# Kernel tuning notes

Hardware: AMD Instinct MI355X
Metric: run time of the kernel (lower is better)

The kernel has to match this reference:

```python
import jax, jax.numpy as jnp
import numpy as np

N_NODES = 50000
N_EDGES = 800000
NUM_GRAPHS = 128
FEAT = 128
HID = 64
NUM_LAYERS = 3
OUT = 2
K = 30
LATENT = HID * NUM_LAYERS + 1  # 193 = conv1 kernel size & stride


def _lin(k, i, o):
    s = 1.0 / np.sqrt(i)
    return jax.random.uniform(k, (i, o), jnp.float32, -s, s)


def setup_inputs() -> dict:
    key = jax.random.key(0)
    ks = jax.random.split(key, 16)
    x = jax.random.normal(ks[0], (N_NODES, FEAT), jnp.float32)
    edge_index = jax.random.randint(ks[1], (2, N_EDGES), 0, N_NODES, dtype=jnp.int64)
    batch = jnp.sort(jax.random.randint(ks[2], (N_NODES,), 0, NUM_GRAPHS, dtype=jnp.int64))
    w0 = _lin(ks[3], FEAT, HID); b0 = jnp.zeros((HID,), jnp.float32)
    w1 = _lin(ks[4], HID, HID);  b1 = jnp.zeros((HID,), jnp.float32)
    w2 = _lin(ks[5], HID, HID);  b2 = jnp.zeros((HID,), jnp.float32)
    w3 = _lin(ks[6], HID, 1);    b3 = jnp.zeros((1,), jnp.float32)
    conv1_w = jax.random.normal(ks[7], (16, 1, LATENT), jnp.float32) * (1.0 / np.sqrt(LATENT))
    conv1_b = jnp.zeros((16,), jnp.float32)
    conv2_w = jax.random.normal(ks[8], (32, 16, 5), jnp.float32) * (1.0 / np.sqrt(16 * 5))
    conv2_b = jnp.zeros((32,), jnp.float32)
    dense_dim = (int((K - 2) / 2 + 1) - 5 + 1) * 32  # 352
    lin1_w = _lin(ks[9], dense_dim, 256); lin1_b = jnp.zeros((256,), jnp.float32)
    lin2_w = _lin(ks[10], 256, OUT);      lin2_b = jnp.zeros((OUT,), jnp.float32)
    return dict(x=x, edge_index=edge_index, batch=batch,
                w0=w0, b0=b0, w1=w1, b1=b1, w2=w2, b2=b2, w3=w3, b3=b3,
                conv1_w=conv1_w, conv1_b=conv1_b, conv2_w=conv2_w, conv2_b=conv2_b,
                lin1_w=lin1_w, lin1_b=lin1_b, lin2_w=lin2_w, lin2_b=lin2_b)


def _gcn(h_in, w, b, src, dst, norm, n):
    # GCNConv: out_i = sum_j d_i^-1/2 d_j^-1/2 (x_j W) over A+I, plus bias
    h = h_in @ w
    msg = h[src] * norm[:, None]  # gather over edges (incl. self loops)
    return jax.ops.segment_sum(msg, dst, num_segments=n) + b


def _sort_pool(x, batch, k, g):
    # per-graph descending sort on last channel, top-k, zero-pad
    n, d = x.shape
    order = jnp.lexsort((-x[:, -1], batch))  # primary: batch asc, secondary: last feat desc
    xs, bs = x[order], batch[order]
    counts = jax.ops.segment_sum(jnp.ones((n,), jnp.int32), batch, num_segments=g)
    starts = jnp.cumsum(counts) - counts
    rank = jnp.arange(n) - starts[bs]
    slot = jnp.where(rank < k, rank, k)  # overflow nodes dumped in slot k (discarded)
    out = jnp.zeros((g, k + 1, d), x.dtype).at[bs, slot].set(xs)
    return out[:, :k].reshape(g, k * d)


def _conv1d(z, w, stride):
    return jax.lax.conv_general_dilated(z, w, window_strides=(stride,), padding='VALID',
                                        dimension_numbers=('NCH', 'OIH', 'NCH'))


def reference(x, edge_index, batch, w0, b0, w1, b1, w2, b2, w3, b3,
              conv1_w, conv1_b, conv2_w, conv2_b, lin1_w, lin1_b, lin2_w, lin2_b):
    n = x.shape[0]
    loop = jnp.arange(n, dtype=edge_index.dtype)
    src = jnp.concatenate([edge_index[0], loop])
    dst = jnp.concatenate([edge_index[1], loop])
    deg = jax.ops.segment_sum(jnp.ones_like(src, jnp.float32), dst, num_segments=n)
    dinv = jnp.where(deg > 0, jax.lax.rsqrt(deg), 0.0)
    norm = dinv[src] * dinv[dst]

    h1 = jnp.tanh(_gcn(x,  w0, b0, src, dst, norm, n))
    h2 = jnp.tanh(_gcn(h1, w1, b1, src, dst, norm, n))
    h3 = jnp.tanh(_gcn(h2, w2, b2, src, dst, norm, n))
    h4 = jnp.tanh(_gcn(h3, w3, b3, src, dst, norm, n))
    hcat = jnp.concatenate([h1, h2, h3, h4], axis=-1)  # [N, 193]

    p = _sort_pool(hcat, batch, K, NUM_GRAPHS)  # [G, K*193]
    z = p[:, None, :]                                   # [G, 1, K*193]
    z = jax.nn.relu(_conv1d(z, conv1_w, LATENT) + conv1_b[None, :, None])  # [G,16,K]
    g, c, l = z.shape
    z = z.reshape(g, c, l // 2, 2).max(axis=-1)         # MaxPool1d(2,2) -> [G,16,15]
    z = jax.nn.relu(_conv1d(z, conv2_w, 1) + conv2_b[None, :, None])       # [G,32,11]
    z = z.reshape(g, -1)                                # [G,352]
    z = jax.nn.relu(z @ lin1_w + lin1_b)
    # dropout is identity in eval mode
    return z @ lin2_w + lin2_b
```

## Files before the change

kernel.cpp:

```cpp
#include <hip/hip_runtime.h>
#include <math.h>

#define NGRAPH 128
#define KTOP 30
#define LATENT 193
#define HID 64

typedef unsigned short u16;

__global__ void k_zero(int* edeg, int n) {
    int i = blockIdx.x * blockDim.x + threadIdx.x;
    if (i < n) edeg[i] = 0;
}

template <bool SCALE>
__device__ __forceinline__ void gemm_tile(const float* __restrict__ A,
                                          const float* __restrict__ W,
                                          const float* __restrict__ dinv,
                                          float* __restrict__ Hs,
                                          int M, int K, int br,
                                          float (*As)[68], float (*Bs)[68]) {
    int tid = threadIdx.x;
    int tx = tid & 15, ty = tid >> 4;
    int kA = (tid & 7) * 4;
    int rA = tid >> 3;
    int kB = tid >> 3;
    int cB = (tid & 7) * 8;
    float c[4][4] = {};
    for (int k0 = 0; k0 < K; k0 += 32) {
#pragma unroll
        for (int it = 0; it < 2; ++it) {
            int row = it * 32 + rA;
            int grow = br + row;
            float4 v = make_float4(0.f, 0.f, 0.f, 0.f);
            if (grow < M) v = *(const float4*)(A + (size_t)grow * K + k0 + kA);
            As[kA + 0][row] = v.x;
            As[kA + 1][row] = v.y;
            As[kA + 2][row] = v.z;
            As[kA + 3][row] = v.w;
        }
        {
            const float* wp = W + (size_t)(k0 + kB) * 64 + cB;
            float4 v0 = *(const float4*)(wp);
            float4 v1 = *(const float4*)(wp + 4);
            *(float4*)&Bs[kB][cB] = v0;
            *(float4*)&Bs[kB][cB + 4] = v1;
        }
        __syncthreads();
#pragma unroll
        for (int kk = 0; kk < 32; ++kk) {
            float4 a4 = *(const float4*)&As[kk][ty * 4];
            float4 b4 = *(const float4*)&Bs[kk][tx * 4];
            c[0][0] += a4.x * b4.x; c[0][1] += a4.x * b4.y; c[0][2] += a4.x * b4.z; c[0][3] += a4.x * b4.w;
            c[1][0] += a4.y * b4.x; c[1][1] += a4.y * b4.y; c[1][2] += a4.y * b4.z; c[1][3] += a4.y * b4.w;
            c[2][0] += a4.z * b4.x; c[2][1] += a4.z * b4.y; c[2][2] += a4.z * b4.z; c[2][3] += a4.z * b4.w;
            c[3][0] += a4.w * b4.x; c[3][1] += a4.w * b4.y; c[3][2] += a4.w * b4.z; c[3][3] += a4.w * b4.w;
        }
        __syncthreads();
    }
#pragma unroll
    for (int i = 0; i < 4; i++) {
        int row = br + ty * 4 + i;
        if (row >= M) continue;
        float d = SCALE ? dinv[row] : 1.f;
        float4 o;
        o.x = c[i][0] * d; o.y = c[i][1] * d; o.z = c[i][2] * d; o.w = c[i][3] * d;
        *(float4*)(Hs + (size_t)row * HID + tx * 4) = o;
    }
}

__global__ __launch_bounds__(256) void k_gemm_hist(
        const float* __restrict__ A, const float* __restrict__ W,
        float* __restrict__ Hs, int M, int K, int NG,
        const int* __restrict__ dst, const int* __restrict__ batch,
        int* edeg, u16* __restrict__ rank, int* starts,
        int E, int n, int NH) {
    __shared__ float As[32][68];
    __shared__ float Bs[32][68];
    int bid = blockIdx.x;
    if ((bid & 1) == 0) {
        int gid = bid >> 1;
        if (gid >= NG) return;
        gemm_tile<false>(A, W, nullptr, Hs, M, K, gid * 64, As, Bs);
    } else {
        int fid = bid >> 1;
        if (fid >= NH) return;
        int t = threadIdx.x;
        int gi = fid * 256 + t;
        if (gi < n) {
            int b = batch[gi];
            if (gi == 0) {
                for (int g = 0; g <= b; g++) starts[g] = 0;
            } else {
                int pb = batch[gi - 1];
                for (int g = pb + 1; g <= b; g++) starts[g] = gi;
            }
            if (gi == n - 1) {
                for (int g = b + 1; g <= NGRAPH; g++) starts[g] = n;
            }
        }
        int base = fid * 1024;
#pragma unroll
        for (int k = 0; k < 4; k++) {
            int e = base + k * 256 + t;
            if (e < E) {
                int d = dst[e];
                rank[e] = (u16)atomicAdd(&edeg[d], 1);
            }
        }
    }
}

__global__ void k_scan1(const int* __restrict__ edeg, int* offs, int* bsum,
                        float* dinv, int n) {
    __shared__ int s[256];
    int t = threadIdx.x;
    int gi = blockIdx.x * 256 + t;
    int v = (gi < n) ? edeg[gi] : 0;
    if (gi < n) dinv[gi] = rsqrtf((float)(v + 1));
    s[t] = v;
    __syncthreads();
    for (int o = 1; o < 256; o <<= 1) {
        int add = (t >= o) ? s[t - o] : 0;
        __syncthreads();
        s[t] += add;
        __syncthreads();
    }
    if (gi < n) offs[gi] = s[t] - v;
    if (t == 255) bsum[blockIdx.x] = s[255];
}

__global__ void k_scan23(int* offs, const int* __restrict__ bsum,
                         int n, int E, int nb) {
    __shared__ int s[256];
    int t = threadIdx.x;
    int bid = blockIdx.x;
    int v = (t < nb) ? bsum[t] : 0;
    s[t] = v;
    __syncthreads();
    for (int o = 1; o < 256; o <<= 1) {
        int add = (t >= o) ? s[t - o] : 0;
        __syncthreads();
        s[t] += add;
        __syncthreads();
    }
    int boffv = (bid == 0) ? 0 : s[bid - 1];
    int gi = bid * 256 + t;
    if (gi < n) offs[gi] += boffv;
    if (gi == 0) offs[n] = E;
}

__global__ __launch_bounds__(256) void k_fill_scale(
        const int* __restrict__ src, const int* __restrict__ dst,
        const u16* __restrict__ rank, const int* __restrict__ offs,
        u16* __restrict__ csr, int E, int NF,
        float* __restrict__ Hs, const float* __restrict__ dinv, int n) {
    int bid = blockIdx.x;
    if (bid < NF) {
        int t = bid * 256 + threadIdx.x;
        int e0 = t * 4;
        if (e0 + 4 <= E) {
            int4 s4 = *(const int4*)(src + e0);
            int4 d4 = *(const int4*)(dst + e0);
            uint2 rv = *(const uint2*)(rank + e0);
            csr[offs[d4.x] + (rv.x & 0xffff)] = (u16)s4.x;
            csr[offs[d4.y] + (rv.x >> 16)]    = (u16)s4.y;
            csr[offs[d4.z] + (rv.y & 0xffff)] = (u16)s4.z;
            csr[offs[d4.w] + (rv.y >> 16)]    = (u16)s4.w;
        } else {
            for (int e = e0; e < E; e++)
                csr[offs[dst[e]] + rank[e]] = (u16)src[e];
        }
    } else {
        int idx = (bid - NF) * 256 + threadIdx.x;
        if (idx < n * HID) Hs[idx] *= dinv[idx >> 6];
    }
}

__global__ __launch_bounds__(256) void k_gemm(const float* __restrict__ A,
                                              const float* __restrict__ W,
                                              const float* __restrict__ dinv,
                                              float* __restrict__ Hs,
                                              int M, int K) {
    __shared__ float As[32][68];
    __shared__ float Bs[32][68];
    gemm_tile<true>(A, W, dinv, Hs, M, K, blockIdx.x * 64, As, Bs);
}

template <bool FUSE_TS>
__global__ __launch_bounds__(256) void k_agg(const float* __restrict__ Hs,
                                             const u16* __restrict__ csr,
                                             const int* __restrict__ offs,
                                             const float* __restrict__ dinv,
                                             const float* __restrict__ b,
                                             float* __restrict__ H, int n,
                                             const float* __restrict__ w3,
                                             float* __restrict__ ts) {
    int wid = threadIdx.x >> 6;
    int lane = threadIdx.x & 63;
    int node = blockIdx.x * 4 + wid;
    if (node >= n) return;
    float d = dinv[node];
    float acc = Hs[(size_t)node * HID + lane];
    int s = offs[node], e = offs[node + 1];
    int i = s;
    int ahead = (s + 7) & ~7;
    if (ahead > e) ahead = e;
    for (; i < ahead; i++) acc += Hs[(size_t)csr[i] * HID + lane];
    for (; i + 8 <= e; i += 8) {
        uint4 c8 = *(const uint4*)(csr + i);
        float v0 = Hs[(size_t)(c8.x & 0xffff) * HID + lane];
        float v1 = Hs[(size_t)(c8.x >> 16)    * HID + lane];
        float v2 = Hs[(size_t)(c8.y & 0xffff) * HID + lane];
        float v3 = Hs[(size_t)(c8.y >> 16)    * HID + lane];
        float v4 = Hs[(size_t)(c8.z & 0xffff) * HID + lane];
        float v5 = Hs[(size_t)(c8.z >> 16)    * HID + lane];
        float v6 = Hs[(size_t)(c8.w & 0xffff) * HID + lane];
        float v7 = Hs[(size_t)(c8.w >> 16)    * HID + lane];
        acc += ((v0 + v1) + (v2 + v3)) + ((v4 + v5) + (v6 + v7));
    }
    for (; i < e; i++) acc += Hs[(size_t)csr[i] * HID + lane];
    float h = tanhf(acc * d + b[lane]);
    H[(size_t)node * HID + lane] = h;
    if (FUSE_TS) {
        float v = h * w3[lane];
        for (int o = 32; o > 0; o >>= 1) v += __shfl_down(v, o, 64);
        if (lane == 0) ts[node] = v * d;
    }
}

__global__ __launch_bounds__(1024) void k_select_tail(
        const float* __restrict__ h1, const float* __restrict__ h2,
        const float* __restrict__ h3, const float* __restrict__ ts,
        const u16* __restrict__ csr, const int* __restrict__ offs,
        const float* __restrict__ dinv, const float* __restrict__ b3,
        const int* __restrict__ starts,
        const float* __restrict__ c1w, const float* __restrict__ c1b,
        const float* __restrict__ c2w, const float* __restrict__ c2b,
        const float* __restrict__ l1w, const float* __restrict__ l1b,
        const float* __restrict__ l2w, const float* __restrict__ l2b,
        float* __restrict__ out) {
    __shared__ float p[KTOP * LATENT];
    __shared__ float w1s[16 * LATENT];
    __shared__ float w2s[32 * 16 * 5];
    __shared__ float vv[2048];
    __shared__ int   pr[2048];
    __shared__ int   sel_s[KTOP];
    __shared__ float zpart[960];
    __shared__ float z1[16 * KTOP];
    __shared__ float z1p[16 * 15];
    __shared__ float flat[352];
    __shared__ float part[1024];
    __shared__ float y1[256];
    int g = blockIdx.x;
    int t = threadIdx.x;
    int s = starts[g];
    int c = starts[g + 1] - s;
    if (c > 2048) c = 2048;

    for (int i = t; i < 16 * LATENT; i += 1024) w1s[i] = c1w[i];
    for (int i = t; i < 32 * 16 * 5; i += 1024) w2s[i] = c2w[i];
    if (t < KTOP) sel_s[t] = -1;

    float bb = b3[0];
    for (int i = t; i < c; i += 1024) {
        int node = s + i;
        float acc = ts[node];
        int es = offs[node], ee = offs[node + 1];
        for (int j = es; j < ee; j++) acc += ts[csr[j]];
        vv[i] = tanhf(acc * dinv[node] + bb);
    }
    __syncthreads();

    int chalf = c >> 1;
    for (int i2 = t; i2 < 2 * c; i2 += 1024) {
        int i = i2 >> 1, half = i2 & 1;
        float vi = vv[i];
        int j0 = half ? chalf : 0;
        int j1 = half ? c : chalf;
        int r = 0;
        for (int j = j0; j < j1; j++) {
            float vj = vv[j];
            r += (vj > vi) || (vj == vi && j < i);
        }
        pr[i2] = r;
    }
    __syncthreads();
    for (int i = t; i < c; i += 1024) {
        int r = pr[2 * i] + pr[2 * i + 1];
        if (r < KTOP) sel_s[r] = s + i;
    }
    __syncthreads();

    for (int i = t; i < KTOP * LATENT; i += 1024) {
        int slot = i / LATENT;
        int j = i - slot * LATENT;
        int node = sel_s[slot];
        float v = 0.f;
        if (node >= 0) {
            if (j < 64)       v = h1[(size_t)node * HID + j];
            else if (j < 128) v = h2[(size_t)node * HID + j - 64];
            else if (j < 192) v = h3[(size_t)node * HID + j - 128];
            else              v = vv[node - s];
        }
        p[i] = v;
    }
    __syncthreads();
    if (t < 960) {
        int to = (t < 480) ? t : t - 480;
        int half = (t < 480) ? 0 : 1;
        int ch = to / KTOP, tt = to - ch * KTOP;
        const float* wp = &w1s[ch * LATENT];
        const float* pp = &p[tt * LATENT];
        int j0 = half ? 96 : 0;
        int j1 = half ? LATENT : 96;
        float sa = 0.f;
        for (int j = j0; j < j1; j++) sa += pp[j] * wp[j];
        zpart[t] = sa;
    }
    __syncthreads();
    if (t < 480) {
        int ch = t / KTOP, tt = t - ch * KTOP;
        z1[ch * KTOP + tt] = fmaxf(zpart[t] + zpart[480 + t] + c1b[ch], 0.f);
    }
    __syncthreads();
    if (t < 16 * 15) {
        int ch = t / 15, tt = t - ch * 15;
        z1p[t] = fmaxf(z1[ch * KTOP + 2 * tt], z1[ch * KTOP + 2 * tt + 1]);
    }
    __syncthreads();
    if (t < 32 * 11) {
        int c2 = t / 11, tt = t - c2 * 11;
        float sa = c2b[c2];
        for (int c1i = 0; c1i < 16; c1i++) {
            const float* wp = &w2s[(c2 * 16 + c1i) * 5];
            const float* zp = &z1p[c1i * 15 + tt];
#pragma unroll
            for (int dt = 0; dt < 5; dt++) sa += zp[dt] * wp[dt];
        }
        flat[c2 * 11 + tt] = fmaxf(sa, 0.f);
    }
    __syncthreads();
    {
        int o = t & 255, ch = t >> 8;
        int i0 = ch * 88, i1 = i0 + 88;
        float sa = 0.f;
        for (int i = i0; i < i1; i++) sa += flat[i] * l1w[(size_t)i * 256 + o];
        part[t] = sa;
    }
    __syncthreads();
    if (t < 256)
        y1[t] = fmaxf(part[t] + part[256 + t] + part[512 + t] + part[768 + t] + l1b[t], 0.f);
    __syncthreads();
    if (t < 128) {
        int o = t >> 6, lane = t & 63;
        float sa = 0.f;
        for (int i = lane; i < 256; i += 64) sa += y1[i] * l2w[(size_t)i * 2 + o];
        for (int off = 32; off > 0; off >>= 1) sa += __shfl_down(sa, off, 64);
        if (lane == 0) out[g * 2 + o] = sa + l2b[o];
    }
}

static inline char* align256(char* p) {
    return (char*)(((uintptr_t)p + 255) & ~(uintptr_t)255);
}

extern "C" void kernel_launch(void* const* d_in, const int* in_sizes, int n_in,
                              void* d_out, int out_size, void* d_ws, size_t ws_size,
                              hipStream_t stream) {
    const float* x     = (const float*)d_in[0];
    const int*  eidx   = (const int*)d_in[1];
    const int*  batch  = (const int*)d_in[2];
    const float* w0    = (const float*)d_in[3];
    const float* b0    = (const float*)d_in[4];
    const float* w1    = (const float*)d_in[5];
    const float* b1    = (const float*)d_in[6];
    const float* w2    = (const float*)d_in[7];
    const float* b2    = (const float*)d_in[8];
    const float* w3    = (const float*)d_in[9];
    const float* b3    = (const float*)d_in[10];
    const float* c1w   = (const float*)d_in[11];
    const float* c1b   = (const float*)d_in[12];
    const float* c2w   = (const float*)d_in[13];
    const float* c2b   = (const float*)d_in[14];
    const float* l1w   = (const float*)d_in[15];
    const float* l1b   = (const float*)d_in[16];
    const float* l2w   = (const float*)d_in[17];
    const float* l2b   = (const float*)d_in[18];

    int N = in_sizes[2];
    int E = in_sizes[1] / 2;
    int K0 = in_sizes[0] / N;
    const int* esrc = eidx;
    const int* edst = eidx + E;

    char* w = (char*)d_ws;
    float* dinv  = (float*)w;             w = align256(w + (size_t)N * 4);
    int*   edeg  = (int*)w;               w = align256(w + (size_t)N * 4);
    int*   offs  = (int*)w;               w = align256(w + (size_t)(N + 1) * 4);
    int*   bsum  = (int*)w;               w = align256(w + 1024);
    float* ts    = (float*)w;             w = align256(w + (size_t)N * 4);
    int* starts  = (int*)w;               w = align256(w + (NGRAPH + 1) * 4);
    u16* rank    = (u16*)w;               w = align256(w + (size_t)E * 2);
    u16* csr     = (u16*)w;               w = align256(w + (size_t)E * 2);
    float* Hs    = (float*)w;             w = align256(w + (size_t)N * HID * 4);
    float* h1    = (float*)w;             w = align256(w + (size_t)N * HID * 4);
    float* h2    = (float*)w;             w = align256(w + (size_t)N * HID * 4);
    float* h3    = (float*)w;             w = align256(w + (size_t)N * HID * 4);

    int nb = (N + 255) / 256;
    int NG = (N + 63) / 64;
    int NH = (E + 1023) / 1024;
    int NF = (E / 4 + 255) / 256 + 1;
    int NS = ((size_t)N * HID + 255) / 256;
    int agg_grid = (N + 3) / 4;

    k_zero<<<nb, 256, 0, stream>>>(edeg, N);

    int g1 = 2 * (NG > NH ? NG : NH);
    k_gemm_hist<<<g1, 256, 0, stream>>>(x, w0, Hs, N, K0, NG,
                                        edst, batch, edeg, rank, starts, E, N, NH);

    k_scan1<<<nb, 256, 0, stream>>>(edeg, offs, bsum, dinv, N);
    k_scan23<<<nb, 256, 0, stream>>>(offs, bsum, N, E, nb);

    k_fill_scale<<<NF + NS, 256, 0, stream>>>(esrc, edst, rank, offs, csr, E, NF,
                                              Hs, dinv, N);

    k_agg<false><<<agg_grid, 256, 0, stream>>>(Hs, csr, offs, dinv, b0, h1, N, nullptr, nullptr);
    k_gemm<<<NG, 256, 0, stream>>>(h1, w1, dinv, Hs, N, HID);
    k_agg<false><<<agg_grid, 256, 0, stream>>>(Hs, csr, offs, dinv, b1, h2, N, nullptr, nullptr);
    k_gemm<<<NG, 256, 0, stream>>>(h2, w2, dinv, Hs, N, HID);
    k_agg<true><<<agg_grid, 256, 0, stream>>>(Hs, csr, offs, dinv, b2, h3, N, w3, ts);

    k_select_tail<<<NGRAPH, 1024, 0, stream>>>(h1, h2, h3, ts, csr, offs, dinv, b3,
                                               starts,
                                               c1w, c1b, c2w, c2b,
                                               l1w, l1b, l2w, l2b,
                                               (float*)d_out);
}
```

Measured before the change: 282.2 us.

## Defer first-layer dinv scaling into aggregation and split neighbor loop into two streams

The separate pass that scaled Hs by dinv after the first GEMM is removed. The first aggregation now multiplies each gathered neighbor row and the self row by dinv on the fly, which saves one full read and write of the N x 64 buffer. The aggregation loop is also rewritten to walk two halves of each node's neighbor list at once, reading indices as scalars, to expose more independent loads. The cost is an extra scattered dinv load per edge in layer one and the loss of the vectorized uint4 index loads.

```diff
diff --git a/kernel.cpp b/kernel.cpp
--- a/kernel.cpp
+++ b/kernel.cpp
@@ -150,30 +150,24 @@
     if (gi == 0) offs[n] = E;
 }
 
-__global__ __launch_bounds__(256) void k_fill_scale(
-        const int* __restrict__ src, const int* __restrict__ dst,
-        const u16* __restrict__ rank, const int* __restrict__ offs,
-        u16* __restrict__ csr, int E, int NF,
-        float* __restrict__ Hs, const float* __restrict__ dinv, int n) {
-    int bid = blockIdx.x;
-    if (bid < NF) {
-        int t = bid * 256 + threadIdx.x;
-        int e0 = t * 4;
-        if (e0 + 4 <= E) {
-            int4 s4 = *(const int4*)(src + e0);
-            int4 d4 = *(const int4*)(dst + e0);
-            uint2 rv = *(const uint2*)(rank + e0);
-            csr[offs[d4.x] + (rv.x & 0xffff)] = (u16)s4.x;
-            csr[offs[d4.y] + (rv.x >> 16)]    = (u16)s4.y;
-            csr[offs[d4.z] + (rv.y & 0xffff)] = (u16)s4.z;
-            csr[offs[d4.w] + (rv.y >> 16)]    = (u16)s4.w;
-        } else {
-            for (int e = e0; e < E; e++)
-                csr[offs[dst[e]] + rank[e]] = (u16)src[e];
-        }
+__global__ __launch_bounds__(256) void k_fill(const int* __restrict__ src,
+                                              const int* __restrict__ dst,
+                                              const u16* __restrict__ rank,
+                                              const int* __restrict__ offs,
+                                              u16* __restrict__ csr, int E) {
+    int t = blockIdx.x * 256 + threadIdx.x;
+    int e0 = t * 4;
+    if (e0 + 4 <= E) {
+        int4 s4 = *(const int4*)(src + e0);
+        int4 d4 = *(const int4*)(dst + e0);
+        uint2 rv = *(const uint2*)(rank + e0);
+        csr[offs[d4.x] + (rv.x & 0xffff)] = (u16)s4.x;
+        csr[offs[d4.y] + (rv.x >> 16)]    = (u16)s4.y;
+        csr[offs[d4.z] + (rv.y & 0xffff)] = (u16)s4.z;
+        csr[offs[d4.w] + (rv.y >> 16)]    = (u16)s4.w;
     } else {
-        int idx = (bid - NF) * 256 + threadIdx.x;
-        if (idx < n * HID) Hs[idx] *= dinv[idx >> 6];
+        for (int e = e0; e < E; e++)
+            csr[offs[dst[e]] + rank[e]] = (u16)src[e];
     }
 }
 
@@ -187,7 +181,7 @@
     gemm_tile<true>(A, W, dinv, Hs, M, K, blockIdx.x * 64, As, Bs);
 }
 
-template <bool FUSE_TS>
+template <bool DEFER, bool FUSE_TS>
 __global__ __launch_bounds__(256) void k_agg(const float* __restrict__ Hs,
                                              const u16* __restrict__ csr,
                                              const int* __restrict__ offs,
@@ -202,24 +196,58 @@
     if (node >= n) return;
     float d = dinv[node];
     float acc = Hs[(size_t)node * HID + lane];
-    int s = offs[node], e = offs[node + 1];
-    int i = s;
-    int ahead = (s + 7) & ~7;
-    if (ahead > e) ahead = e;
-    for (; i < ahead; i++) acc += Hs[(size_t)csr[i] * HID + lane];
-    for (; i + 8 <= e; i += 8) {
-        uint4 c8 = *(const uint4*)(csr + i);
-        float v0 = Hs[(size_t)(c8.x & 0xffff) * HID + lane];
-        float v1 = Hs[(size_t)(c8.x >> 16)    * HID + lane];
-        float v2 = Hs[(size_t)(c8.y & 0xffff) * HID + lane];
-        float v3 = Hs[(size_t)(c8.y >> 16)    * HID + lane];
-        float v4 = Hs[(size_t)(c8.z & 0xffff) * HID + lane];
-        float v5 = Hs[(size_t)(c8.z >> 16)    * HID + lane];
-        float v6 = Hs[(size_t)(c8.w & 0xffff) * HID + lane];
-        float v7 = Hs[(size_t)(c8.w >> 16)    * HID + lane];
-        acc += ((v0 + v1) + (v2 + v3)) + ((v4 + v5) + (v6 + v7));
-    }
-    for (; i < e; i++) acc += Hs[(size_t)csr[i] * HID + lane];
+    if (DEFER) acc *= d;
+    int s0 = offs[node], e1 = offs[node + 1];
+    int mid = s0 + ((e1 - s0) >> 1);
+    int iA = s0, iB = mid;
+    while (iA + 8 <= mid && iB + 8 <= e1) {
+        float pa = 0.f, pb = 0.f;
+#pragma unroll
+        for (int k = 0; k < 8; k++) {
+            int uA = csr[iA + k];
+            int uB = csr[iB + k];
+            float vA = Hs[(size_t)uA * HID + lane];
+            float vB = Hs[(size_t)uB * HID + lane];
+            if (DEFER) { vA *= dinv[uA]; vB *= dinv[uB]; }
+            pa += vA; pb += vB;
+        }
+        acc += pa + pb;
+        iA += 8; iB += 8;
+    }
+    for (; iA + 8 <= mid; iA += 8) {
+        float pa = 0.f;
+#pragma unroll
+        for (int k = 0; k < 8; k++) {
+            int u = csr[iA + k];
+            float v = Hs[(size_t)u * HID + lane];
+            if (DEFER) v *= dinv[u];
+            pa += v;
+        }
+        acc += pa;
+    }
+    for (; iA < mid; ++iA) {
+        int u = csr[iA];
+        float v = Hs[(size_t)u * HID + lane];
+        if (DEFER) v *= dinv[u];
+        acc += v;
+    }
+    for (; iB + 8 <= e1; iB += 8) {
+        float pb = 0.f;
+#pragma unroll
+        for (int k = 0; k < 8; k++) {
+            int u = csr[iB + k];
+            float v = Hs[(size_t)u * HID + lane];
+            if (DEFER) v *= dinv[u];
+            pb += v;
+        }
+        acc += pb;
+    }
+    for (; iB < e1; ++iB) {
+        int u = csr[iB];
+        float v = Hs[(size_t)u * HID + lane];
+        if (DEFER) v *= dinv[u];
+        acc += v;
+    }
     float h = tanhf(acc * d + b[lane]);
     H[(size_t)node * HID + lane] = h;
     if (FUSE_TS) {
@@ -411,8 +439,6 @@
     int nb = (N + 255) / 256;
     int NG = (N + 63) / 64;
     int NH = (E + 1023) / 1024;
-    int NF = (E / 4 + 255) / 256 + 1;
-    int NS = ((size_t)N * HID + 255) / 256;
     int agg_grid = (N + 3) / 4;
 
     k_zero<<<nb, 256, 0, stream>>>(edeg, N);
@@ -424,14 +450,13 @@
     k_scan1<<<nb, 256, 0, stream>>>(edeg, offs, bsum, dinv, N);
     k_scan23<<<nb, 256, 0, stream>>>(offs, bsum, N, E, nb);
 
-    k_fill_scale<<<NF + NS, 256, 0, stream>>>(esrc, edst, rank, offs, csr, E, NF,
-                                              Hs, dinv, N);
-
-    k_agg<false><<<agg_grid, 256, 0, stream>>>(Hs, csr, offs, dinv, b0, h1, N, nullptr, nullptr);
+    k_fill<<<(E / 4 + 255) / 256 + 1, 256, 0, stream>>>(esrc, edst, rank, offs, csr, E);
+
+    k_agg<true, false><<<agg_grid, 256, 0, stream>>>(Hs, csr, offs, dinv, b0, h1, N, nullptr, nullptr);
     k_gemm<<<NG, 256, 0, stream>>>(h1, w1, dinv, Hs, N, HID);
-    k_agg<false><<<agg_grid, 256, 0, stream>>>(Hs, csr, offs, dinv, b1, h2, N, nullptr, nullptr);
+    k_agg<false, false><<<agg_grid, 256, 0, stream>>>(Hs, csr, offs, dinv, b1, h2, N, nullptr, nullptr);
     k_gemm<<<NG, 256, 0, stream>>>(h2, w2, dinv, Hs, N, HID);
-    k_agg<true><<<agg_grid, 256, 0, stream>>>(Hs, csr, offs, dinv, b2, h3, N, w3, ts);
+    k_agg<false, true><<<agg_grid, 256, 0, stream>>>(Hs, csr, offs, dinv, b2, h3, N, w3, ts);
 
     k_select_tail<<<NGRAPH, 1024, 0, stream>>>(h1, h2, h3, ts, csr, offs, dinv, b3,
                                                starts,
```

Result: no change. 282.8 us (+0.2%).
